# Kernel optimization log

Measured on AMD Instinct MI355X. Metric: run time of the kernel, lower is better.

The kernel has to match this reference:

```python
import jax, jax.numpy as jnp
import numpy as np

B, N, K_NEIGHBORS = 8, 2048, 16

def setup_inputs() -> dict:
    key = jax.random.key(0)
    k1, k2, k3 = jax.random.split(key, 3)
    distance_matrix = jax.random.uniform(k1, (B, N, N), dtype=jnp.float32)
    time_window_compatibility = jax.random.randint(k2, (B, N, N), 0, 2).astype(jnp.int32)
    depot = jax.random.randint(k3, (B, N), 0, 2).astype(jnp.int32)
    # graph.max_dist: per-batch max pairwise distance, broadcastable over [B,N,N]
    max_dist = jnp.max(distance_matrix.reshape(B, -1), axis=1).reshape(B, 1, 1)
    return {
        "distance_matrix": distance_matrix,
        "max_dist": max_dist,
        "time_window_compatibility": time_window_compatibility,
        "depot": depot,
        "num_neighbors_encoder": K_NEIGHBORS,
    }


def reference(distance_matrix, max_dist, time_window_compatibility, depot, num_neighbors_encoder):
    """Faithful JAX port of Actor.compute_encoder_mask.

    distance_matrix:            [B, N, N] float
    max_dist:                   [B, 1, 1] float
    time_window_compatibility:  [B, N, N] int 0/1
    depot:                      [B, N]    int 0/1
    num_neighbors_encoder:      python int (K)
    returns mask:               [B, N, N] float 0/1
    """
    dtype = distance_matrix.dtype
    b, n, _ = distance_matrix.shape

    twnc = (1 - time_window_compatibility).astype(dtype)          # time-window NON-compatibility
    diag = jnp.eye(n, dtype=dtype)                                  # [N,N], broadcasts over batch
    m = ((twnc + diag) > 0).astype(dtype)                           # blocked pairs for KNN

    # Push blocked pairs far away, then take K smallest distances per row.
    dist = distance_matrix * (1.0 - m) + m * max_dist * 10.0
    k = min(n, int(num_neighbors_encoder))
    neighbors_index = jax.lax.top_k(-dist, k)[1]                    # [B, N, K] smallest-dist indices

    # neighbors_mask[b,i,j] = 1 iff j is among the K nearest neighbors of i.
    bi = jnp.arange(b)[:, None, None]
    ii = jnp.arange(n)[None, :, None]
    neighbors_mask = jnp.zeros((b, n, n), dtype).at[bi, ii, neighbors_index].add(1.0)

    m2 = (twnc == 0).astype(dtype)                                  # time-window compatible pairs
    neighbs_time_mask = neighbors_mask * m2

    depot_f = depot.astype(dtype)
    depot_mask = ((depot_f[:, None, :] + depot_f[:, :, None]) > 0).astype(dtype)

    mask = ((neighbs_time_mask + depot_mask + diag) > 0).astype(dtype)
    return mask
```

## Files before the change

kernel.cpp:

```cpp
#include <hip/hip_runtime.h>
#include <stdint.h>

#define NN 2048
#define TPB 256
#define WPB 4
#define KNB 16
#define CAP 128
#define CAPPAD (CAP + 8)

static constexpr unsigned long long EXCL = ~0ull;
static constexpr unsigned long long T0KEY = ((unsigned long long)0x3D400000u) << 11;

#define WAVE_LDS_SYNC() asm volatile("s_waitcnt lgkmcnt(0)" ::: "memory")

__global__ __launch_bounds__(TPB, 8) void encoder_mask_kernel(
    const float* __restrict__ D,
    const int*   __restrict__ TWC,
    const int*   __restrict__ depot,
    float*       __restrict__ out)
{
    const int t    = threadIdx.x;
    const int w    = t >> 6;
    const int lane = t & 63;
    const int row  = blockIdx.x * WPB + w;
    const int b    = row >> 11;
    const int i    = row & (NN - 1);

    const int* deprow = depot + b * NN;
    float*     orow   = out + (size_t)row * NN;
    const int  depot_i = deprow[i];

    if (depot_i != 0) {
        const float4 ones = make_float4(1.f, 1.f, 1.f, 1.f);
        #pragma unroll
        for (int k = 0; k < 8; ++k)
            reinterpret_cast<float4*>(orow)[lane + 64 * k] = ones;
        return;
    }

    __shared__ unsigned int       selq[WPB][512];
    __shared__ unsigned long long cand[WPB][CAPPAD];
    __shared__ int                cnt[WPB];

    if (lane == 0) cnt[w] = 0;
    cand[w][lane]      = EXCL;
    cand[w][lane + 64] = EXCL;
    if (lane < CAPPAD - 128) cand[w][128 + lane] = EXCL;

    #pragma unroll
    for (int k = 0; k < 8; ++k) {
        const int idx = lane + 64 * k;
        const int4 dp = reinterpret_cast<const int4*>(deprow)[idx];
        unsigned int m = (dp.x != 0 ? 0x00000001u : 0u)
                       | (dp.y != 0 ? 0x00000100u : 0u)
                       | (dp.z != 0 ? 0x00010000u : 0u)
                       | (dp.w != 0 ? 0x01000000u : 0u);
        if (idx == (i >> 2)) m |= 1u << (8 * (i & 3));
        selq[w][idx] = m;
    }

    const float* drow = D   + (size_t)row * NN;
    const int*   trow = TWC + (size_t)row * NN;

    #pragma unroll 2
    for (int k = 0; k < 8; ++k) {
        const int idx = lane + 64 * k;
        const float4 d4 = reinterpret_cast<const float4*>(drow)[idx];
        const int4   c4 = reinterpret_cast<const int4*>(trow)[idx];
        const int jb = 4 * idx;
        const float dd[4] = {d4.x, d4.y, d4.z, d4.w};
        const int   cc[4] = {c4.x, c4.y, c4.z, c4.w};
        unsigned long long kk[4];
        int nl = 0;
        #pragma unroll
        for (int q = 0; q < 4; ++q) {
            const int j = jb + q;
            const bool excl = (cc[q] == 0) | (j == i);
            kk[q] = excl ? EXCL
                         : ((((unsigned long long)__float_as_uint(dd[q])) << 11) |
                            (unsigned long long)(unsigned)j);
            nl += (kk[q] < T0KEY) ? 1 : 0;
        }
        if (nl > 0) {
            int p = atomicAdd(&cnt[w], nl);
            #pragma unroll
            for (int q = 0; q < 4; ++q) {
                if (kk[q] < T0KEY) {
                    if (p < CAP) cand[w][p] = kk[q];
                    ++p;
                }
            }
        }
    }
    WAVE_LDS_SYNC();

    const int c = cnt[w];

    if (c >= KNB && c <= CAP) {
        const unsigned long long k0 = cand[w][lane];
        const unsigned long long k1 = cand[w][lane + 64];
        int r0 = 0, r1 = 0;
        const int cround = (c + 7) & ~7;
        #pragma unroll 1
        for (int q = 0; q < cround; q += 8) {
            const ulonglong2 a0 = *reinterpret_cast<const ulonglong2*>(&cand[w][q]);
            const ulonglong2 a1 = *reinterpret_cast<const ulonglong2*>(&cand[w][q + 2]);
            const ulonglong2 a2 = *reinterpret_cast<const ulonglong2*>(&cand[w][q + 4]);
            const ulonglong2 a3 = *reinterpret_cast<const ulonglong2*>(&cand[w][q + 6]);
            r0 += (a0.x < k0) + (a0.y < k0) + (a1.x < k0) + (a1.y < k0)
                + (a2.x < k0) + (a2.y < k0) + (a3.x < k0) + (a3.y < k0);
            r1 += (a0.x < k1) + (a0.y < k1) + (a1.x < k1) + (a1.y < k1)
                + (a2.x < k1) + (a2.y < k1) + (a3.x < k1) + (a3.y < k1);
        }
        unsigned char* selb = reinterpret_cast<unsigned char*>(&selq[w][0]);
        if (lane      < c && r0 < KNB) selb[(int)(k0 & 2047u)] = 1;
        if (lane + 64 < c && r1 < KNB) selb[(int)(k1 & 2047u)] = 1;
    } else {
        unsigned long long glast = 0ull;
        #pragma unroll 1
        for (int it = 0; it < KNB; ++it) {
            unsigned long long lmin = EXCL;
            #pragma unroll 1
            for (int k = 0; k < 8; ++k) {
                const int idx = lane + 64 * k;
                const float4 d4 = reinterpret_cast<const float4*>(drow)[idx];
                const int4   c4 = reinterpret_cast<const int4*>(trow)[idx];
                const int jb = 4 * idx;
                const float dd[4] = {d4.x, d4.y, d4.z, d4.w};
                const int   cc[4] = {c4.x, c4.y, c4.z, c4.w};
                #pragma unroll
                for (int q = 0; q < 4; ++q) {
                    const int j = jb + q;
                    const bool excl = (cc[q] == 0) | (j == i);
                    const unsigned long long kq = excl ? EXCL
                        : ((((unsigned long long)__float_as_uint(dd[q])) << 11) |
                           (unsigned long long)(unsigned)j);
                    const bool ok = (it == 0) | (kq > glast);
                    if (ok && kq < lmin) lmin = kq;
                }
            }
            #pragma unroll
            for (int off = 32; off >= 1; off >>= 1) {
                const unsigned long long o = __shfl_xor(lmin, off);
                lmin = (o < lmin) ? o : lmin;
            }
            if (lmin == EXCL) break;
            if (lane == 0)
                reinterpret_cast<unsigned char*>(&selq[w][0])[(int)(lmin & 2047u)] = 1;
            glast = lmin;
        }
    }
    WAVE_LDS_SYNC();

    unsigned int sv[8];
    #pragma unroll
    for (int k = 0; k < 8; ++k) sv[k] = selq[w][lane + 64 * k];

    #pragma unroll
    for (int k = 0; k < 8; ++k) {
        const unsigned int s = sv[k];
        float4 o;
        o.x = (s & 0x000000ffu) ? 1.f : 0.f;
        o.y = (s & 0x0000ff00u) ? 1.f : 0.f;
        o.z = (s & 0x00ff0000u) ? 1.f : 0.f;
        o.w = (s & 0xff000000u) ? 1.f : 0.f;
        reinterpret_cast<float4*>(orow)[lane + 64 * k] = o;
    }
}

extern "C" void kernel_launch(void* const* d_in, const int* in_sizes, int n_in,
                              void* d_out, int out_size, void* d_ws, size_t ws_size,
                              hipStream_t stream) {
    const float* D     = (const float*)d_in[0];
    const int*   TWC   = (const int*)d_in[2];
    const int*   depot = (const int*)d_in[3];

    float* outp = (float*)d_out;
    const int rows = in_sizes[3];

    encoder_mask_kernel<<<rows / WPB, TPB, 0, stream>>>(D, TWC, depot, outp);
}
```

Before: 55.35 us.

## Gather time-window flags only for near candidates and defer depot merge to output

The distance row is preloaded into registers, and the time-window row is no longer streamed in full. A compatibility flag is read only for entries whose distance falls under the threshold, and each hit is appended to the candidate list with its own LDS atomic. The depot OR is moved into the final write loop, so the selection bitmap starts as zero plus the diagonal. This cuts global read traffic roughly in half in the common path, but brings scattered 4-byte gathers, per-element atomics and higher register pressure. The fallback path still rereads the full TWC row.

```diff
diff --git a/kernel.cpp b/kernel.cpp
--- a/kernel.cpp
+++ b/kernel.cpp
@@ -9,6 +9,7 @@
 #define CAPPAD (CAP + 8)
 
 static constexpr unsigned long long EXCL = ~0ull;
+static constexpr float T0F = 0.046875f;
 static constexpr unsigned long long T0KEY = ((unsigned long long)0x3D400000u) << 11;
 
 #define WAVE_LDS_SYNC() asm volatile("s_waitcnt lgkmcnt(0)" ::: "memory")
@@ -38,6 +39,14 @@
         return;
     }
 
+    const float* drow = D   + (size_t)row * NN;
+    const int*   trow = TWC + (size_t)row * NN;
+
+    float4 dv[8];
+    #pragma unroll
+    for (int k = 0; k < 8; ++k)
+        dv[k] = reinterpret_cast<const float4*>(drow)[lane + 64 * k];
+
     __shared__ unsigned int       selq[WPB][512];
     __shared__ unsigned long long cand[WPB][CAPPAD];
     __shared__ int                cnt[WPB];
@@ -46,48 +55,26 @@
     cand[w][lane]      = EXCL;
     cand[w][lane + 64] = EXCL;
     if (lane < CAPPAD - 128) cand[w][128 + lane] = EXCL;
+    #pragma unroll
+    for (int k = 0; k < 8; ++k) selq[w][lane + 64 * k] = 0u;
+    if (lane == 0)
+        reinterpret_cast<unsigned char*>(&selq[w][0])[i] = 1;
+    WAVE_LDS_SYNC();
 
     #pragma unroll
     for (int k = 0; k < 8; ++k) {
-        const int idx = lane + 64 * k;
-        const int4 dp = reinterpret_cast<const int4*>(deprow)[idx];
-        unsigned int m = (dp.x != 0 ? 0x00000001u : 0u)
-                       | (dp.y != 0 ? 0x00000100u : 0u)
-                       | (dp.z != 0 ? 0x00010000u : 0u)
-                       | (dp.w != 0 ? 0x01000000u : 0u);
-        if (idx == (i >> 2)) m |= 1u << (8 * (i & 3));
-        selq[w][idx] = m;
-    }
-
-    const float* drow = D   + (size_t)row * NN;
-    const int*   trow = TWC + (size_t)row * NN;
-
-    #pragma unroll 2
-    for (int k = 0; k < 8; ++k) {
-        const int idx = lane + 64 * k;
-        const float4 d4 = reinterpret_cast<const float4*>(drow)[idx];
-        const int4   c4 = reinterpret_cast<const int4*>(trow)[idx];
-        const int jb = 4 * idx;
-        const float dd[4] = {d4.x, d4.y, d4.z, d4.w};
-        const int   cc[4] = {c4.x, c4.y, c4.z, c4.w};
-        unsigned long long kk[4];
-        int nl = 0;
+        const int jb = 4 * (lane + 64 * k);
+        const float dd[4] = {dv[k].x, dv[k].y, dv[k].z, dv[k].w};
         #pragma unroll
         for (int q = 0; q < 4; ++q) {
             const int j = jb + q;
-            const bool excl = (cc[q] == 0) | (j == i);
-            kk[q] = excl ? EXCL
-                         : ((((unsigned long long)__float_as_uint(dd[q])) << 11) |
-                            (unsigned long long)(unsigned)j);
-            nl += (kk[q] < T0KEY) ? 1 : 0;
-        }
-        if (nl > 0) {
-            int p = atomicAdd(&cnt[w], nl);
-            #pragma unroll
-            for (int q = 0; q < 4; ++q) {
-                if (kk[q] < T0KEY) {
-                    if (p < CAP) cand[w][p] = kk[q];
-                    ++p;
+            if ((dd[q] < T0F) & (j != i)) {
+                if (trow[j] != 0) {
+                    const unsigned long long kk =
+                        ((((unsigned long long)__float_as_uint(dd[q])) << 11) |
+                         (unsigned long long)(unsigned)j);
+                    const int p = atomicAdd(&cnt[w], 1);
+                    if (p < CAP) cand[w][p] = kk;
                 }
             }
         }
@@ -152,19 +139,17 @@
     }
     WAVE_LDS_SYNC();
 
-    unsigned int sv[8];
-    #pragma unroll
-    for (int k = 0; k < 8; ++k) sv[k] = selq[w][lane + 64 * k];
-
     #pragma unroll
     for (int k = 0; k < 8; ++k) {
-        const unsigned int s = sv[k];
+        const int idx = lane + 64 * k;
+        const int4 dp = reinterpret_cast<const int4*>(deprow)[idx];
+        const unsigned int s = selq[w][idx];
         float4 o;
-        o.x = (s & 0x000000ffu) ? 1.f : 0.f;
-        o.y = (s & 0x0000ff00u) ? 1.f : 0.f;
-        o.z = (s & 0x00ff0000u) ? 1.f : 0.f;
-        o.w = (s & 0xff000000u) ? 1.f : 0.f;
-        reinterpret_cast<float4*>(orow)[lane + 64 * k] = o;
+        o.x = ((s & 0x000000ffu) | (dp.x != 0)) ? 1.f : 0.f;
+        o.y = ((s & 0x0000ff00u) | (dp.y != 0)) ? 1.f : 0.f;
+        o.z = ((s & 0x00ff0000u) | (dp.z != 0)) ? 1.f : 0.f;
+        o.w = ((s & 0xff000000u) | (dp.w != 0)) ? 1.f : 0.f;
+        reinterpret_cast<float4*>(orow)[idx] = o;
     }
 }
 
```

Result: slower. 68.60 us (+23.9%).
